# Performance work log

Hardware: AMD Instinct MI355X
Metric: run time of the kernel (lower is better)

The kernel has to match this reference:

```python
import jax, jax.numpy as jnp
import numpy as np

N = 100000
IN_C = 128
HID = 32   # 2*out_channels
OUT = 16
NEG_SLOPE = 0.2


def gat_layer(x, src, dst, n, W, a_src, a_dst, b):
    # x: [n, Cin] -> h: [n, Cout]
    h = x @ W
    alpha_s = h @ a_src  # [n]
    alpha_d = h @ a_dst  # [n]
    e = jax.nn.leaky_relu(alpha_s[src] + alpha_d[dst], NEG_SLOPE)  # [E]
    # softmax over edges grouped by destination node (self-loops ensure no empty groups)
    m = jax.ops.segment_max(e, dst, num_segments=n)
    ex = jnp.exp(e - m[dst])
    s = jax.ops.segment_sum(ex, dst, num_segments=n)
    alpha = ex / s[dst]  # [E]
    out = jax.ops.segment_sum(h[src] * alpha[:, None], dst, num_segments=n)
    return out + b


def setup_inputs() -> dict:
    key = jax.random.key(0)
    ks = jax.random.split(key, 16)
    x = jax.random.normal(ks[0], (N, IN_C), dtype=jnp.float32)
    edge_index = jax.random.randint(ks[1], (2, 1600000), 0, N, dtype=jnp.int64)

    def glorot(k, shape):
        fan = shape[0] + (shape[1] if len(shape) > 1 else 1)
        return jax.random.normal(k, shape, dtype=jnp.float32) * jnp.sqrt(2.0 / fan)

    return {
        "x": x,
        "edge_index": edge_index,
        "W1": glorot(ks[2], (IN_C, HID)),
        "a1_src": glorot(ks[3], (HID,)),
        "a1_dst": glorot(ks[4], (HID,)),
        "b1": jnp.zeros((HID,), dtype=jnp.float32),
        "W_mu": glorot(ks[5], (HID, OUT)),
        "a_mu_src": glorot(ks[6], (OUT,)),
        "a_mu_dst": glorot(ks[7], (OUT,)),
        "b_mu": jnp.zeros((OUT,), dtype=jnp.float32),
        "W_ls": glorot(ks[8], (HID, OUT)),
        "a_ls_src": glorot(ks[9], (OUT,)),
        "a_ls_dst": glorot(ks[10], (OUT,)),
        "b_ls": jnp.zeros((OUT,), dtype=jnp.float32),
    }


def reference(x, edge_index, W1, a1_src, a1_dst, b1,
              W_mu, a_mu_src, a_mu_dst, b_mu,
              W_ls, a_ls_src, a_ls_dst, b_ls):
    n = x.shape[0]
    # PyG GATConv default: add self-loops
    loop = jnp.arange(n, dtype=edge_index.dtype)
    src = jnp.concatenate([edge_index[0], loop])
    dst = jnp.concatenate([edge_index[1], loop])

    h = jax.nn.relu(gat_layer(x, src, dst, n, W1, a1_src, a1_dst, b1))
    mu = gat_layer(h, src, dst, n, W_mu, a_mu_src, a_mu_dst, b_mu)
    logstd = gat_layer(h, src, dst, n, W_ls, a_ls_src, a_ls_dst, b_ls)
    return (mu, logstd)
```

## Files before the change

kernel.cpp:

```cpp
#include <hip/hip_runtime.h>
#include <hip/hip_bf16.h>
#include <hip/hip_fp16.h>

typedef unsigned int u32;
typedef unsigned short u16;

__device__ __forceinline__ float lrelu(float v) {
    return v > 0.f ? v : 0.2f * v;
}

__device__ __forceinline__ float4 ldq_h16(const u16* __restrict__ row, int q) {
    uint2 u = ((const uint2*)row)[q];
    __half2 a = *(__half2*)&u.x;
    __half2 b = *(__half2*)&u.y;
    float2 fa = __half22float2(a);
    float2 fb = __half22float2(b);
    return make_float4(fa.x, fa.y, fb.x, fb.y);
}

__device__ __forceinline__ u32 pack2h(float x, float y) {
    __half2 h = __float22half2_rn(make_float2(x, y));
    return *(u32*)&h;
}

__global__ __launch_bounds__(256) void gemm1_kernel(
    const float* __restrict__ x, const float* __restrict__ W,
    const float* __restrict__ a_src, const float* __restrict__ a_dst,
    u16* __restrict__ h16, float* __restrict__ as_, float* __restrict__ ad_,
    int n)
{
    __shared__ float xs[64][132];
    __shared__ float Wl[128][32];
    __shared__ float asv[32], adv[32];
    int t = threadIdx.x;
    int rb = blockIdx.x * 64;

    for (int i = t; i < 4096; i += 256) Wl[i >> 5][i & 31] = W[i];
    if (t < 32) { asv[t] = a_src[t]; adv[t] = a_dst[t]; }
    for (int i = t; i < 2048; i += 256) {
        int row = i >> 5, seg = i & 31;
        float4 v = make_float4(0.f, 0.f, 0.f, 0.f);
        if (rb + row < n)
            v = ((const float4*)(x + (size_t)(rb + row) * 128))[seg];
        int c = seg * 4;
        xs[row][c + 0] = v.x; xs[row][c + 1] = v.y;
        xs[row][c + 2] = v.z; xs[row][c + 3] = v.w;
    }
    __syncthreads();

    int tr = t >> 3;
    int tc = t & 7;
    float acc[2][4];
#pragma unroll
    for (int i = 0; i < 2; i++)
#pragma unroll
        for (int j = 0; j < 4; j++) acc[i][j] = 0.f;

#pragma unroll 4
    for (int k = 0; k < 128; k++) {
        float x0 = xs[tr][k];
        float x1 = xs[tr + 32][k];
        float4 wv = *(const float4*)&Wl[k][tc * 4];
        acc[0][0] += x0 * wv.x; acc[0][1] += x0 * wv.y;
        acc[0][2] += x0 * wv.z; acc[0][3] += x0 * wv.w;
        acc[1][0] += x1 * wv.x; acc[1][1] += x1 * wv.y;
        acc[1][2] += x1 * wv.z; acc[1][3] += x1 * wv.w;
    }

#pragma unroll
    for (int i = 0; i < 2; i++) {
        int r = rb + tr + i * 32;
        if (r < n) {
            uint2 p;
            p.x = pack2h(acc[i][0], acc[i][1]);
            p.y = pack2h(acc[i][2], acc[i][3]);
            *(uint2*)&h16[(size_t)r * 32 + tc * 4] = p;
        }
        float ps = 0.f, pd = 0.f;
#pragma unroll
        for (int j = 0; j < 4; j++) {
            int c = tc * 4 + j;
            ps += acc[i][j] * asv[c];
            pd += acc[i][j] * adv[c];
        }
        for (int m = 1; m < 8; m <<= 1) {
            ps += __shfl_xor(ps, m, 64);
            pd += __shfl_xor(pd, m, 64);
        }
        if (tc == 0 && r < n) { as_[r] = ps; ad_[r] = pd; }
    }
}

#define PCHUNK 4096
#define NW 256
__global__ __launch_bounds__(256) void partition_kernel(
    const int* __restrict__ srcI, const int* __restrict__ dstI,
    u32* __restrict__ pairs, u32* __restrict__ bcur,
    int E, int wsz, int cap)
{
    __shared__ u32 lcount[NW];
    __shared__ u32 lbase[NW];
    int t = threadIdx.x;
    for (int chunk = blockIdx.x * PCHUNK; chunk < E; chunk += gridDim.x * PCHUNK) {
        lcount[t] = 0;
        __syncthreads();
        u32 pk[16]; int wv[16]; u32 rk[16]; bool val[16];
#pragma unroll
        for (int k = 0; k < 16; k++) {
            int i = chunk + k * 256 + t;
            val[k] = i < E;
            if (val[k]) {
                u32 s = (u32)srcI[i];
                u32 d = (u32)dstI[i];
                wv[k] = d / (u32)wsz;
                u32 dloc = d - (u32)wv[k] * (u32)wsz;
                pk[k] = (dloc << 17) | s;
                rk[k] = atomicAdd(&lcount[wv[k]], 1u);
            }
        }
        __syncthreads();
        if (lcount[t] > 0)
            lbase[t] = atomicAdd(&bcur[t], lcount[t]);
        __syncthreads();
#pragma unroll
        for (int k = 0; k < 16; k++) {
            if (val[k]) {
                u32 pos = lbase[wv[k]] + rk[k];
                if (pos < (u32)cap)
                    pairs[(size_t)wv[k] * cap + pos] = pk[k];
            }
        }
        __syncthreads();
    }
}

__global__ void wbase_kernel(const u32* __restrict__ bcur,
                             u32* __restrict__ wbase, int n, int wsz, int cap)
{
    __shared__ u32 ts[NW];
    int t = threadIdx.x;
    int wlo = t * wsz;
    int wnodes = n - wlo; if (wnodes < 0) wnodes = 0; if (wnodes > wsz) wnodes = wsz;
    u32 cnt = bcur[t]; if (cnt > (u32)cap) cnt = (u32)cap;
    u32 tot = cnt + (u32)wnodes;
    ts[t] = tot; __syncthreads();
    for (int o = 1; o < NW; o <<= 1) {
        u32 y = (t >= o) ? ts[t - o] : 0u;
        __syncthreads();
        ts[t] += y;
        __syncthreads();
    }
    wbase[t] = ts[t] - tot;
}

__global__ __launch_bounds__(256) void csr_window_kernel(
    const u32* __restrict__ pairs, const u32* __restrict__ bcur,
    const u32* __restrict__ wbase,
    u32* __restrict__ rowS, u32* __restrict__ deg, int* __restrict__ srcS,
    int n, int wsz, int cap)
{
    __shared__ u32 dw[512];
    __shared__ u32 cw[512];
    __shared__ u32 ts[256];
    int grp = blockIdx.x;
    int t = threadIdx.x;
    int wlo = grp * wsz;
    int wnodes = n - wlo; if (wnodes < 0) wnodes = 0; if (wnodes > wsz) wnodes = wsz;
    u32 cnt = bcur[grp]; if (cnt > (u32)cap) cnt = (u32)cap;
    size_t base = (size_t)grp * cap;

    dw[t] = 0; dw[t + 256] = 0;
    __syncthreads();
    for (u32 i = t; i < cnt; i += 256)
        atomicAdd(&dw[pairs[base + i] >> 17], 1u);
    __syncthreads();

    int i0 = 2 * t, i1 = 2 * t + 1;
    u32 e0 = (i0 < wnodes) ? dw[i0] + 1u : 0u;
    u32 e1 = (i1 < wnodes) ? dw[i1] + 1u : 0u;
    ts[t] = e0 + e1;
    __syncthreads();
    for (int o = 1; o < 256; o <<= 1) {
        u32 y = (t >= o) ? ts[t - o] : 0u;
        __syncthreads();
        ts[t] += y;
        __syncthreads();
    }
    u32 off = wbase[grp] + ts[t] - (e0 + e1);
    if (i0 < wnodes) {
        u32 dgi = dw[i0];
        cw[i0] = off;
        rowS[wlo + i0] = off;
        deg[wlo + i0] = dgi;
        srcS[off + dgi] = wlo + i0;
    }
    u32 off1 = off + e0;
    if (i1 < wnodes) {
        u32 dgi = dw[i1];
        cw[i1] = off1;
        rowS[wlo + i1] = off1;
        deg[wlo + i1] = dgi;
        srcS[off1 + dgi] = wlo + i1;
    }
    __syncthreads();

    for (u32 i = t; i < cnt; i += 256) {
        u32 pr = pairs[base + i];
        u32 pos = atomicAdd(&cw[pr >> 17], 1u);
        srcS[pos] = (int)(pr & 0x1FFFFu);
    }
}

__global__ __launch_bounds__(256) void l1_fused_kernel(
    const u32* __restrict__ rowS, const u32* __restrict__ deg,
    const int* __restrict__ srcS,
    const float* __restrict__ as_, const float* __restrict__ ad_,
    const u16* __restrict__ h16, const float* __restrict__ b1,
    float* __restrict__ h1r, int n)
{
    int d = blockIdx.x * 16 + (threadIdx.x >> 4);
    if (d >= n) return;
    int l  = threadIdx.x & 15;
    int e2 = l >> 3;
    int q  = l & 7;
    int gb = (threadIdx.x & 63) & 48;

    int beg = (int)rowS[d];
    int end = beg + (int)deg[d] + 1;
    float adv = ad_[d];

    float wsum = 0.f;
    float4 acc = make_float4(0.f, 0.f, 0.f, 0.f);

    for (int tb = beg; tb < end; tb += 16) {
        int j = tb + l;
        bool valid = j < end;
        int s = valid ? srcS[j] : 0;
        float p = valid ? __expf(fminf(lrelu(as_[s] + adv), 60.f)) : 0.f;
        int cnt = end - tb; if (cnt > 16) cnt = 16;
        for (int jj = 0; jj < cnt; jj += 2) {
            int idx = jj + e2;
            int sj  = __shfl(s, gb + idx, 64);
            float w = __shfl(p, gb + idx, 64);
            if (idx >= cnt) w = 0.f;
            wsum += w;
            float4 hv = ldq_h16(h16 + (size_t)sj * 32, q);
            acc.x += w * hv.x; acc.y += w * hv.y;
            acc.z += w * hv.z; acc.w += w * hv.w;
        }
    }
    wsum  += __shfl_xor(wsum, 8, 64);
    acc.x += __shfl_xor(acc.x, 8, 64);
    acc.y += __shfl_xor(acc.y, 8, 64);
    acc.z += __shfl_xor(acc.z, 8, 64);
    acc.w += __shfl_xor(acc.w, 8, 64);
    if (l < 8) {
        float inv = 1.f / wsum;
        float4 r;
        r.x = fmaxf(acc.x * inv + b1[4 * q + 0], 0.f);
        r.y = fmaxf(acc.y * inv + b1[4 * q + 1], 0.f);
        r.z = fmaxf(acc.z * inv + b1[4 * q + 2], 0.f);
        r.w = fmaxf(acc.w * inv + b1[4 * q + 3], 0.f);
        *(float4*)&h1r[(size_t)d * 32 + 4 * q] = r;
    }
}

__global__ __launch_bounds__(256) void gemm2_kernel(
    const float* __restrict__ h1r,
    const float* __restrict__ Wm, const float* __restrict__ Wl_,
    const float* __restrict__ ams, const float* __restrict__ amd,
    const float* __restrict__ alsb, const float* __restrict__ ald,
    u16* __restrict__ hmhl16, float2* __restrict__ attn2,
    float* __restrict__ amud, float* __restrict__ alsd, int n)
{
    __shared__ float hs[16][33];
    __shared__ float Wms[32][16], Wls[32][16];
    __shared__ float amsv[16], amdv[16], alsv[16], aldv[16];
    int t = threadIdx.x;
    int rb = blockIdx.x * 16;

    for (int i = t; i < 512; i += 256) {
        int k = i >> 4, c = i & 15;
        Wms[k][c] = Wm[i];
        Wls[k][c] = Wl_[i];
    }
    if (t < 16) {
        amsv[t] = ams[t]; amdv[t] = amd[t];
        alsv[t] = alsb[t]; aldv[t] = ald[t];
    }
    for (int i = t; i < 512; i += 256) {
        int r = i >> 5, k = i & 31;
        int gr = rb + r;
        hs[r][k] = (gr < n) ? h1r[(size_t)gr * 32 + k] : 0.f;
    }
    __syncthreads();

    int tr = t >> 4;
    int c = t & 15;
    float accm = 0.f, accl = 0.f;
#pragma unroll
    for (int k = 0; k < 32; k++) {
        float hv = hs[tr][k];
        accm += hv * Wms[k][c];
        accl += hv * Wls[k][c];
    }
    int r = rb + tr;
    if (r < n) {
        hmhl16[(size_t)r * 32 + c]      = __half_as_ushort(__float2half(accm));
        hmhl16[(size_t)r * 32 + 16 + c] = __half_as_ushort(__float2half(accl));
    }
    float pms = accm * amsv[c], pmd = accm * amdv[c];
    float pls = accl * alsv[c], pld = accl * aldv[c];
    for (int m = 1; m < 16; m <<= 1) {
        pms += __shfl_xor(pms, m, 64);
        pmd += __shfl_xor(pmd, m, 64);
        pls += __shfl_xor(pls, m, 64);
        pld += __shfl_xor(pld, m, 64);
    }
    if (c == 0 && r < n) {
        attn2[r] = make_float2(pms, pls);
        amud[r] = pmd;
        alsd[r] = pld;
    }
}

__global__ __launch_bounds__(256) void l2_fused_kernel(
    const u32* __restrict__ rowS, const u32* __restrict__ deg,
    const int* __restrict__ srcS,
    const float2* __restrict__ attn2,
    const float* __restrict__ amud, const float* __restrict__ alsd,
    const u16* __restrict__ hmhl16,
    const float* __restrict__ bm, const float* __restrict__ bl,
    float* __restrict__ out, int n)
{
    int d = blockIdx.x * 16 + (threadIdx.x >> 4);
    if (d >= n) return;
    int l  = threadIdx.x & 15;
    int e2 = l >> 3;
    int q  = l & 7;
    int gb = (threadIdx.x & 63) & 48;
    bool isMu = q < 4;

    int beg = (int)rowS[d];
    int end = beg + (int)deg[d] + 1;
    float amdv = amud[d], aldv = alsd[d];

    float wsum = 0.f;
    float4 acc = make_float4(0.f, 0.f, 0.f, 0.f);

    for (int tb = beg; tb < end; tb += 16) {
        int j = tb + l;
        bool valid = j < end;
        int s = valid ? srcS[j] : 0;
        float2 a2 = valid ? attn2[s] : make_float2(0.f, 0.f);
        float pm = valid ? __expf(fminf(lrelu(a2.x + amdv), 60.f)) : 0.f;
        float pl = valid ? __expf(fminf(lrelu(a2.y + aldv), 60.f)) : 0.f;
        int cnt = end - tb; if (cnt > 16) cnt = 16;
        for (int jj = 0; jj < cnt; jj += 2) {
            int idx = jj + e2;
            int sj    = __shfl(s, gb + idx, 64);
            float pmj = __shfl(pm, gb + idx, 64);
            float plj = __shfl(pl, gb + idx, 64);
            float w = isMu ? pmj : plj;
            if (idx >= cnt) w = 0.f;
            wsum += w;
            float4 hv = ldq_h16(hmhl16 + (size_t)sj * 32, q);
            acc.x += w * hv.x; acc.y += w * hv.y;
            acc.z += w * hv.z; acc.w += w * hv.w;
        }
    }
    wsum  += __shfl_xor(wsum, 8, 64);
    acc.x += __shfl_xor(acc.x, 8, 64);
    acc.y += __shfl_xor(acc.y, 8, 64);
    acc.z += __shfl_xor(acc.z, 8, 64);
    acc.w += __shfl_xor(acc.w, 8, 64);
    if (l < 8) {
        float inv = 1.f / wsum;
        if (q < 4) {
            float4 r;
            r.x = acc.x * inv + bm[4 * q + 0];
            r.y = acc.y * inv + bm[4 * q + 1];
            r.z = acc.z * inv + bm[4 * q + 2];
            r.w = acc.w * inv + bm[4 * q + 3];
            *(float4*)&out[(size_t)d * 16 + 4 * q] = r;
        } else {
            int qc = 4 * (q - 4);
            float4 r;
            r.x = acc.x * inv + bl[qc + 0];
            r.y = acc.y * inv + bl[qc + 1];
            r.z = acc.z * inv + bl[qc + 2];
            r.w = acc.w * inv + bl[qc + 3];
            *(float4*)&out[(size_t)n * 16 + (size_t)d * 16 + qc] = r;
        }
    }
}

extern "C" void kernel_launch(void* const* d_in, const int* in_sizes, int n_in,
                              void* d_out, int out_size, void* d_ws, size_t ws_size,
                              hipStream_t stream)
{
    const float* x   = (const float*)d_in[0];
    const int*   ei  = (const int*)d_in[1];
    const float* W1  = (const float*)d_in[2];
    const float* a1s = (const float*)d_in[3];
    const float* a1d = (const float*)d_in[4];
    const float* b1  = (const float*)d_in[5];
    const float* Wm  = (const float*)d_in[6];
    const float* ams = (const float*)d_in[7];
    const float* amd = (const float*)d_in[8];
    const float* bm  = (const float*)d_in[9];
    const float* Wl  = (const float*)d_in[10];
    const float* als = (const float*)d_in[11];
    const float* ald = (const float*)d_in[12];
    const float* bl  = (const float*)d_in[13];

    int n  = in_sizes[0] / 128;
    int E  = in_sizes[1] / 2;
    int Et = E + n;
    int wsz = (n + NW - 1) / NW;
    int cap = E / NW + 3072;
    const int* srcI = ei;
    const int* dstI = ei + E;

    float* ws = (float*)d_ws;
    u16*    h16   = (u16*)ws;
    u16*    hmhl16 = (u16*)(ws + (size_t)16 * n);
    float*  h1r  = ws + (size_t)32 * n;
    u32*    pairs = (u32*)(ws + (size_t)32 * n);
    float*  as_  = ws + (size_t)64 * n;
    float*  ad_  = ws + (size_t)65 * n;
    float2* attn2 = (float2*)(ws + (size_t)64 * n);
    float*  amud = ws + (size_t)66 * n;
    float*  alsd = ws + (size_t)67 * n;
    u32*    deg  = (u32*)(ws + (size_t)68 * n);
    u32*    bcur = (u32*)(ws + (size_t)69 * n);
    u32*    rowS = (u32*)(ws + (size_t)70 * n);
    int*    srcS = (int*)(ws + (size_t)71 * n);
    u32*    wbase = (u32*)(ws + (size_t)71 * n + Et);

    int pgrid = (E + PCHUNK - 1) / PCHUNK;

    hipMemsetAsync(bcur, 0, NW * sizeof(u32), stream);

    gemm1_kernel<<<(n + 63) / 64, 256, 0, stream>>>(x, W1, a1s, a1d, h16, as_, ad_, n);

    partition_kernel<<<pgrid, 256, 0, stream>>>(srcI, dstI, pairs, bcur, E, wsz, cap);
    wbase_kernel<<<1, NW, 0, stream>>>(bcur, wbase, n, wsz, cap);
    csr_window_kernel<<<NW, 256, 0, stream>>>(pairs, bcur, wbase,
                                              rowS, deg, srcS, n, wsz, cap);

    l1_fused_kernel<<<(n + 15) / 16, 256, 0, stream>>>(rowS, deg, srcS, as_, ad_,
                                                       h16, b1, h1r, n);

    gemm2_kernel<<<(n + 15) / 16, 256, 0, stream>>>(h1r, Wm, Wl, ams, amd, als, ald,
                                                    hmhl16, attn2, amud, alsd, n);

    l2_fused_kernel<<<(n + 15) / 16, 256, 0, stream>>>(rowS, deg, srcS,
                                                       attn2, amud, alsd,
                                                       hmhl16, bm, bl,
                                                       (float*)d_out, n);
}
```

Measured before the change: 263.4 us.

## Merge gemm1 with edge partitioning and fold window-base scan into CSR kernel

Combines the layer-1 GEMM and the edge partitioning pass into one launch, with block ranges split by role, so the two independent phases run concurrently and one launch goes away. The single-block window-base prefix scan kernel is removed, and each CSR window block instead recomputes the full 256-entry scan itself. This cuts two kernel launches and their serialization, at the cost of redundant scan work in every CSR block and higher shared-memory use for the partition blocks, which now also reserve the GEMM tiles.

```diff
diff --git a/kernel.cpp b/kernel.cpp
--- a/kernel.cpp
+++ b/kernel.cpp
@@ -23,85 +23,26 @@
     return *(u32*)&h;
 }
 
-__global__ __launch_bounds__(256) void gemm1_kernel(
+#define PCHUNK 4096
+#define NW 256
+
+__global__ __launch_bounds__(256) void g1p_kernel(
     const float* __restrict__ x, const float* __restrict__ W,
     const float* __restrict__ a_src, const float* __restrict__ a_dst,
     u16* __restrict__ h16, float* __restrict__ as_, float* __restrict__ ad_,
-    int n)
+    const int* __restrict__ srcI, const int* __restrict__ dstI,
+    u32* __restrict__ pairs, u32* __restrict__ bcur,
+    int n, int E, int wsz, int cap, int pgrid)
 {
     __shared__ float xs[64][132];
     __shared__ float Wl[128][32];
     __shared__ float asv[32], adv[32];
-    int t = threadIdx.x;
-    int rb = blockIdx.x * 64;
-
-    for (int i = t; i < 4096; i += 256) Wl[i >> 5][i & 31] = W[i];
-    if (t < 32) { asv[t] = a_src[t]; adv[t] = a_dst[t]; }
-    for (int i = t; i < 2048; i += 256) {
-        int row = i >> 5, seg = i & 31;
-        float4 v = make_float4(0.f, 0.f, 0.f, 0.f);
-        if (rb + row < n)
-            v = ((const float4*)(x + (size_t)(rb + row) * 128))[seg];
-        int c = seg * 4;
-        xs[row][c + 0] = v.x; xs[row][c + 1] = v.y;
-        xs[row][c + 2] = v.z; xs[row][c + 3] = v.w;
-    }
-    __syncthreads();
-
-    int tr = t >> 3;
-    int tc = t & 7;
-    float acc[2][4];
-#pragma unroll
-    for (int i = 0; i < 2; i++)
-#pragma unroll
-        for (int j = 0; j < 4; j++) acc[i][j] = 0.f;
-
-#pragma unroll 4
-    for (int k = 0; k < 128; k++) {
-        float x0 = xs[tr][k];
-        float x1 = xs[tr + 32][k];
-        float4 wv = *(const float4*)&Wl[k][tc * 4];
-        acc[0][0] += x0 * wv.x; acc[0][1] += x0 * wv.y;
-        acc[0][2] += x0 * wv.z; acc[0][3] += x0 * wv.w;
-        acc[1][0] += x1 * wv.x; acc[1][1] += x1 * wv.y;
-        acc[1][2] += x1 * wv.z; acc[1][3] += x1 * wv.w;
-    }
-
-#pragma unroll
-    for (int i = 0; i < 2; i++) {
-        int r = rb + tr + i * 32;
-        if (r < n) {
-            uint2 p;
-            p.x = pack2h(acc[i][0], acc[i][1]);
-            p.y = pack2h(acc[i][2], acc[i][3]);
-            *(uint2*)&h16[(size_t)r * 32 + tc * 4] = p;
-        }
-        float ps = 0.f, pd = 0.f;
-#pragma unroll
-        for (int j = 0; j < 4; j++) {
-            int c = tc * 4 + j;
-            ps += acc[i][j] * asv[c];
-            pd += acc[i][j] * adv[c];
-        }
-        for (int m = 1; m < 8; m <<= 1) {
-            ps += __shfl_xor(ps, m, 64);
-            pd += __shfl_xor(pd, m, 64);
-        }
-        if (tc == 0 && r < n) { as_[r] = ps; ad_[r] = pd; }
-    }
-}
-
-#define PCHUNK 4096
-#define NW 256
-__global__ __launch_bounds__(256) void partition_kernel(
-    const int* __restrict__ srcI, const int* __restrict__ dstI,
-    u32* __restrict__ pairs, u32* __restrict__ bcur,
-    int E, int wsz, int cap)
-{
     __shared__ u32 lcount[NW];
     __shared__ u32 lbase[NW];
     int t = threadIdx.x;
-    for (int chunk = blockIdx.x * PCHUNK; chunk < E; chunk += gridDim.x * PCHUNK) {
+
+    if ((int)blockIdx.x < pgrid) {
+        int chunk = blockIdx.x * PCHUNK;
         lcount[t] = 0;
         __syncthreads();
         u32 pk[16]; int wv[16]; u32 rk[16]; bool val[16];
@@ -130,32 +71,69 @@
                     pairs[(size_t)wv[k] * cap + pos] = pk[k];
             }
         }
-        __syncthreads();
-    }
-}
-
-__global__ void wbase_kernel(const u32* __restrict__ bcur,
-                             u32* __restrict__ wbase, int n, int wsz, int cap)
-{
-    __shared__ u32 ts[NW];
-    int t = threadIdx.x;
-    int wlo = t * wsz;
-    int wnodes = n - wlo; if (wnodes < 0) wnodes = 0; if (wnodes > wsz) wnodes = wsz;
-    u32 cnt = bcur[t]; if (cnt > (u32)cap) cnt = (u32)cap;
-    u32 tot = cnt + (u32)wnodes;
-    ts[t] = tot; __syncthreads();
-    for (int o = 1; o < NW; o <<= 1) {
-        u32 y = (t >= o) ? ts[t - o] : 0u;
-        __syncthreads();
-        ts[t] += y;
-        __syncthreads();
-    }
-    wbase[t] = ts[t] - tot;
+        return;
+    }
+
+    int rb = (blockIdx.x - pgrid) * 64;
+
+    for (int i = t; i < 4096; i += 256) Wl[i >> 5][i & 31] = W[i];
+    if (t < 32) { asv[t] = a_src[t]; adv[t] = a_dst[t]; }
+    for (int i = t; i < 2048; i += 256) {
+        int row = i >> 5, seg = i & 31;
+        float4 v = make_float4(0.f, 0.f, 0.f, 0.f);
+        if (rb + row < n)
+            v = ((const float4*)(x + (size_t)(rb + row) * 128))[seg];
+        int c = seg * 4;
+        xs[row][c + 0] = v.x; xs[row][c + 1] = v.y;
+        xs[row][c + 2] = v.z; xs[row][c + 3] = v.w;
+    }
+    __syncthreads();
+
+    int tr = t >> 3;
+    int tc = t & 7;
+    float acc[2][4];
+#pragma unroll
+    for (int i = 0; i < 2; i++)
+#pragma unroll
+        for (int j = 0; j < 4; j++) acc[i][j] = 0.f;
+
+#pragma unroll 4
+    for (int k = 0; k < 128; k++) {
+        float x0 = xs[tr][k];
+        float x1 = xs[tr + 32][k];
+        float4 wv = *(const float4*)&Wl[k][tc * 4];
+        acc[0][0] += x0 * wv.x; acc[0][1] += x0 * wv.y;
+        acc[0][2] += x0 * wv.z; acc[0][3] += x0 * wv.w;
+        acc[1][0] += x1 * wv.x; acc[1][1] += x1 * wv.y;
+        acc[1][2] += x1 * wv.z; acc[1][3] += x1 * wv.w;
+    }
+
+#pragma unroll
+    for (int i = 0; i < 2; i++) {
+        int r = rb + tr + i * 32;
+        if (r < n) {
+            uint2 p;
+            p.x = pack2h(acc[i][0], acc[i][1]);
+            p.y = pack2h(acc[i][2], acc[i][3]);
+            *(uint2*)&h16[(size_t)r * 32 + tc * 4] = p;
+        }
+        float ps = 0.f, pd = 0.f;
+#pragma unroll
+        for (int j = 0; j < 4; j++) {
+            int c = tc * 4 + j;
+            ps += acc[i][j] * asv[c];
+            pd += acc[i][j] * adv[c];
+        }
+        for (int m = 1; m < 8; m <<= 1) {
+            ps += __shfl_xor(ps, m, 64);
+            pd += __shfl_xor(pd, m, 64);
+        }
+        if (tc == 0 && r < n) { as_[r] = ps; ad_[r] = pd; }
+    }
 }
 
 __global__ __launch_bounds__(256) void csr_window_kernel(
     const u32* __restrict__ pairs, const u32* __restrict__ bcur,
-    const u32* __restrict__ wbase,
     u32* __restrict__ rowS, u32* __restrict__ deg, int* __restrict__ srcS,
     int n, int wsz, int cap)
 {
@@ -169,6 +147,22 @@
     u32 cnt = bcur[grp]; if (cnt > (u32)cap) cnt = (u32)cap;
     size_t base = (size_t)grp * cap;
 
+    {
+        int wlo_t = t * wsz;
+        int wn_t = n - wlo_t; if (wn_t < 0) wn_t = 0; if (wn_t > wsz) wn_t = wsz;
+        u32 c_t = bcur[t]; if (c_t > (u32)cap) c_t = (u32)cap;
+        ts[t] = c_t + (u32)wn_t;
+        __syncthreads();
+        for (int o = 1; o < NW; o <<= 1) {
+            u32 y = (t >= o) ? ts[t - o] : 0u;
+            __syncthreads();
+            ts[t] += y;
+            __syncthreads();
+        }
+    }
+    u32 wb = ts[grp] - (cnt + (u32)wnodes);
+    __syncthreads();
+
     dw[t] = 0; dw[t + 256] = 0;
     __syncthreads();
     for (u32 i = t; i < cnt; i += 256)
@@ -186,7 +180,7 @@
         ts[t] += y;
         __syncthreads();
     }
-    u32 off = wbase[grp] + ts[t] - (e0 + e1);
+    u32 off = wb + ts[t] - (e0 + e1);
     if (i0 < wnodes) {
         u32 dgi = dw[i0];
         cw[i0] = off;
@@ -436,17 +430,17 @@
     u32*    bcur = (u32*)(ws + (size_t)69 * n);
     u32*    rowS = (u32*)(ws + (size_t)70 * n);
     int*    srcS = (int*)(ws + (size_t)71 * n);
-    u32*    wbase = (u32*)(ws + (size_t)71 * n + Et);
 
     int pgrid = (E + PCHUNK - 1) / PCHUNK;
+    int gblocks = (n + 63) / 64;
 
     hipMemsetAsync(bcur, 0, NW * sizeof(u32), stream);
 
-    gemm1_kernel<<<(n + 63) / 64, 256, 0, stream>>>(x, W1, a1s, a1d, h16, as_, ad_, n);
-
-    partition_kernel<<<pgrid, 256, 0, stream>>>(srcI, dstI, pairs, bcur, E, wsz, cap);
-    wbase_kernel<<<1, NW, 0, stream>>>(bcur, wbase, n, wsz, cap);
-    csr_window_kernel<<<NW, 256, 0, stream>>>(pairs, bcur, wbase,
+    g1p_kernel<<<pgrid + gblocks, 256, 0, stream>>>(
+        x, W1, a1s, a1d, h16, as_, ad_,
+        srcI, dstI, pairs, bcur, n, E, wsz, cap, pgrid);
+
+    csr_window_kernel<<<NW, 256, 0, stream>>>(pairs, bcur,
                                               rowS, deg, srcS, n, wsz, cap);
 
     l1_fused_kernel<<<(n + 15) / 16, 256, 0, stream>>>(rowS, deg, srcS, as_, ad_,
```

New measurement: 257.0 us. 2.4% less time.
